# Performance work log

Hardware: AMD Instinct MI355X
Metric: run time of the kernel (lower is better)

## Reference

```python
import jax, jax.numpy as jnp
import numpy as np

LN_EPS = 1e-6
L2_EPS = 1e-12


def _l2_normalize(v):
    # tf.nn.l2_normalize: v * rsqrt(max(sum(v^2), eps))
    ss = jnp.sum(v * v, axis=-1, keepdims=True)
    return v * jax.lax.rsqrt(jnp.maximum(ss, L2_EPS))


def setup_inputs() -> dict:
    key = jax.random.key(0)
    k1, k2, k3 = jax.random.split(key, 3)
    B, S, D, V = 4, 2048, 1024, 16384
    x = jax.random.normal(k1, (B, S, D), dtype=jnp.float32)
    dict_w = jax.random.normal(k2, (V, D), dtype=jnp.float32) * (2.0 / (V + D)) ** 0.5  # glorot_normal
    ln_gamma = jnp.ones((D,), dtype=jnp.float32)
    ln_beta = jnp.zeros((D,), dtype=jnp.float32)
    o_w = jax.random.normal(k3, (D, D), dtype=jnp.float32) * (2.0 / (D + D)) ** 0.5
    return {"x": x, "dict_w": dict_w, "ln_gamma": ln_gamma, "ln_beta": ln_beta, "o_w": o_w}


def reference(x, dict_w, ln_gamma, ln_beta, o_w):
    # cosine-sim codebook lookup
    q = _l2_normalize(x)                      # [B,S,D]
    k = _l2_normalize(dict_w)                 # [V,D]
    sim = jnp.einsum('bsd,vd->bsv', q, k)     # [B,S,V]
    word_idx = jnp.argmax(sim, axis=-1)       # [B,S] int
    word_sim = jnp.max(sim, axis=-1)          # [B,S]
    z = dict_w[word_idx]                      # gather codebook rows [B,S,D]
    # straight-through estimator
    e = jax.lax.stop_gradient(z - x) + x
    # layernorm (eps=1e-6)
    mu = jnp.mean(e, axis=-1, keepdims=True)
    var = jnp.mean(jnp.square(e - mu), axis=-1, keepdims=True)
    e_ln = (e - mu) * jax.lax.rsqrt(var + LN_EPS) * ln_gamma + ln_beta
    # output projection (no bias)
    out = jnp.einsum('bsd,de->bse', e_ln, o_w)
    return word_idx, word_sim, out
```

## Files before the change

kernel.cpp:

```cpp
#include <hip/hip_runtime.h>
#include <math.h>

#define D 1024
#define V 16384
#define NROWS 8192
#define NCAND 256
#define DELTA 0.15f

typedef __bf16 bf16_t;
typedef bf16_t bf16x8 __attribute__((ext_vector_type(8)));
typedef float f32x4 __attribute__((ext_vector_type(4)));
typedef int i32x4 __attribute__((ext_vector_type(4)));

__device__ __forceinline__ unsigned int sortable_key(float v) {
    unsigned int b = __float_as_uint(v);
    return (b & 0x80000000u) ? ~b : (b | 0x80000000u);
}
__device__ __forceinline__ float unkey(unsigned int key) {
    unsigned int b = (key & 0x80000000u) ? (key & 0x7FFFFFFFu) : ~key;
    return __uint_as_float(b);
}
__device__ __forceinline__ void split4(float4 v, uint2& hw, uint2& lw) {
    unsigned int u0 = __float_as_uint(v.x), u1 = __float_as_uint(v.y);
    unsigned int u2 = __float_as_uint(v.z), u3 = __float_as_uint(v.w);
    float l0 = v.x - __uint_as_float(u0 & 0xFFFF0000u);
    float l1 = v.y - __uint_as_float(u1 & 0xFFFF0000u);
    float l2 = v.z - __uint_as_float(u2 & 0xFFFF0000u);
    float l3 = v.w - __uint_as_float(u3 & 0xFFFF0000u);
    hw.x = (u0 >> 16) | (u1 & 0xFFFF0000u);
    hw.y = (u2 >> 16) | (u3 & 0xFFFF0000u);
    lw.x = (__float_as_uint(l0) >> 16) | (__float_as_uint(l1) & 0xFFFF0000u);
    lw.y = (__float_as_uint(l2) >> 16) | (__float_as_uint(l3) & 0xFFFF0000u);
}

__device__ __forceinline__ void gload16(const unsigned char* g, unsigned char* s) {
    __builtin_amdgcn_global_load_lds((const __attribute__((address_space(1))) void*)g,
                                     (__attribute__((address_space(3))) void*)s,
                                     16, 0, 0);
}

__global__ __launch_bounds__(256) void prep_kernel(const float* __restrict__ W,
                                                   const float* __restrict__ X,
                                                   float* __restrict__ RK,
                                                   float* __restrict__ RQ,
                                                   float* __restrict__ SA,
                                                   float* __restrict__ SB,
                                                   float* __restrict__ RKS,
                                                   unsigned int* __restrict__ packed,
                                                   unsigned int* __restrict__ count) {
    int tid = threadIdx.x;
    int row = blockIdx.x * 4 + (tid >> 6);
    int lane = tid & 63;
    const float* src = (row < V) ? (W + (size_t)row * D) : (X + (size_t)(row - V) * D);
    const float4* p = (const float4*)src;
    float ss = 0.f, am = 0.f;
#pragma unroll
    for (int i = 0; i < 4; ++i) {
        float4 v = p[lane + 64 * i];
        ss += v.x * v.x + v.y * v.y + v.z * v.z + v.w * v.w;
        am = fmaxf(am, fmaxf(fmaxf(fabsf(v.x), fabsf(v.y)), fmaxf(fabsf(v.z), fabsf(v.w))));
    }
#pragma unroll
    for (int m = 32; m >= 1; m >>= 1) {
        ss += __shfl_xor(ss, m, 64);
        am = fmaxf(am, __shfl_xor(am, m, 64));
    }
    if (lane == 0) {
        float rk = rsqrtf(fmaxf(ss, 1e-12f));
        float s = am * (1.f / 127.f);
        if (row < V) {
            RK[row] = rk;
            SB[row] = s;
            RKS[row] = rk * s;
        } else {
            RQ[row - V] = rk;
            SA[row - V] = s;
            packed[row - V] = 0u;
            count[row - V] = 0u;
        }
    }
}

__global__ __launch_bounds__(256) void pack_i8_kernel(const float* __restrict__ src,
                                                      const float* __restrict__ S,
                                                      unsigned char* __restrict__ dst) {
    int tid = threadIdx.x;
    int row = blockIdx.x;
    int k0 = tid * 4;
    float4 v = *((const float4*)(src + (size_t)row * D) + tid);
    float s = S[row];
    float inv = (s > 0.f) ? (1.f / s) : 0.f;
    int q0 = (int)rintf(v.x * inv), q1 = (int)rintf(v.y * inv);
    int q2 = (int)rintf(v.z * inv), q3 = (int)rintf(v.w * inv);
    q0 = q0 > 127 ? 127 : (q0 < -127 ? -127 : q0);
    q1 = q1 > 127 ? 127 : (q1 < -127 ? -127 : q1);
    q2 = q2 > 127 ? 127 : (q2 < -127 ? -127 : q2);
    q3 = q3 > 127 ? 127 : (q3 < -127 ? -127 : q3);
    unsigned int word = (unsigned int)(q0 & 0xFF) | ((unsigned int)(q1 & 0xFF) << 8) |
                        ((unsigned int)(q2 & 0xFF) << 16) | ((unsigned int)(q3 & 0xFF) << 24);
    int kc = k0 >> 6, kk = k0 & 63;
    int lane = (row & 15) | ((kk >> 4) << 4);
    int j0 = kk & 15;
    size_t idx = ((size_t)(row >> 4) * 16 + kc) * 1024 + lane * 16 + j0;
    *(unsigned int*)(dst + idx) = word;
}

__global__ __launch_bounds__(256, 2) void gemm1_kernel(const unsigned char* __restrict__ Xq,
                                                       const unsigned char* __restrict__ Wq,
                                                       const float* __restrict__ SA,
                                                       const float* __restrict__ RKS,
                                                       unsigned int* __restrict__ packed,
                                                       unsigned int* __restrict__ count,
                                                       ushort* __restrict__ candCol,
                                                       int colBase, int perX) {
    __shared__ __align__(16) unsigned char lds[49152];
    __shared__ float red[128][2];
    __shared__ float gthr[128];

    const int tid = threadIdx.x;
    const int l = tid & 63;
    const int w = tid >> 6;
    const int wy = w >> 1, wx = w & 1;
    const int lin = blockIdx.x;
    const int x = lin & 7;
    const int j = lin >> 3;
    const int rt = j / perX;
    const int ctl = x * perX + (j - rt * perX);
    const int rowBase = rt * 128;
    const int cwLocal = ctl * 256;

    i32x4 acc[4][8];
#pragma unroll
    for (int mt = 0; mt < 4; ++mt)
#pragma unroll
        for (int nt = 0; nt < 8; ++nt) acc[mt][nt] = (i32x4)0;

    const unsigned char* As = Xq + ((size_t)(rt * 8) * 16) * 1024;
    const unsigned char* Bs = Wq + ((size_t)((colBase >> 4) + ctl * 16) * 16) * 1024;

#pragma unroll 1
    for (int kc = 0; kc < 16; kc += 2) {
#pragma unroll
        for (int i = 0; i < 2; ++i) {
            int u = 2 * w + i;
#pragma unroll
            for (int jj = 0; jj < 2; ++jj)
                gload16(As + ((size_t)(u * 16 + kc + jj)) * 1024 + l * 16,
                        lds + (u * 2 + jj) * 1024);
        }
#pragma unroll
        for (int i = 0; i < 4; ++i) {
            int u = 4 * w + i;
#pragma unroll
            for (int jj = 0; jj < 2; ++jj)
                gload16(Bs + ((size_t)(u * 16 + kc + jj)) * 1024 + l * 16,
                        lds + 16384 + (u * 2 + jj) * 1024);
        }
        __syncthreads();
#pragma unroll
        for (int jj = 0; jj < 2; ++jj) {
            i32x4 af[4], bf[8];
#pragma unroll
            for (int mi = 0; mi < 4; ++mi)
                af[mi] = *(const i32x4*)(lds + ((wy * 4 + mi) * 2 + jj) * 1024 + l * 16);
#pragma unroll
            for (int nt = 0; nt < 8; ++nt)
                bf[nt] = *(const i32x4*)(lds + 16384 + ((wx * 8 + nt) * 2 + jj) * 1024 + l * 16);
#pragma unroll
            for (int nt = 0; nt < 8; ++nt)
#pragma unroll
                for (int mi = 0; mi < 4; ++mi)
                    acc[mi][nt] = __builtin_amdgcn_mfma_i32_16x16x64_i8(af[mi], bf[nt], acc[mi][nt], 0, 0, 0);
        }
        __syncthreads();
    }

    const int q = l >> 4, c = l & 15;
    float rk_l[8];
#pragma unroll
    for (int nt = 0; nt < 8; ++nt) rk_l[nt] = RKS[colBase + cwLocal + wx * 128 + nt * 16 + c];
#pragma unroll
    for (int mt = 0; mt < 4; ++mt) {
#pragma unroll
        for (int r = 0; r < 4; ++r) {
            int lrow = wy * 64 + mt * 16 + q * 4 + r;
            float sa = SA[rowBase + lrow];
            float vmax = -1e30f;
#pragma unroll
            for (int nt = 0; nt < 8; ++nt)
                vmax = fmaxf(vmax, (float)acc[mt][nt][r] * sa * rk_l[nt]);
#pragma unroll
            for (int m = 1; m < 16; m <<= 1)
                vmax = fmaxf(vmax, __shfl_xor(vmax, m, 64));
            if (c == 0) red[lrow][wx] = vmax;
        }
    }
    __syncthreads();
    if (tid < 128) {
        float a = fmaxf(red[tid][0], red[tid][1]);
        unsigned int k = sortable_key(a);
        unsigned int old = atomicMax(packed + (rowBase + tid), k);
        unsigned int g = (old > k) ? old : k;
        gthr[tid] = unkey(g) - DELTA;
    }
    __syncthreads();
#pragma unroll
    for (int mt = 0; mt < 4; ++mt) {
#pragma unroll
        for (int r = 0; r < 4; ++r) {
            int lrow = wy * 64 + mt * 16 + q * 4 + r;
            float thr = gthr[lrow];
            int grow = rowBase + lrow;
            float sa = SA[grow];
#pragma unroll
            for (int nt = 0; nt < 8; ++nt) {
                float v = (float)acc[mt][nt][r] * sa * rk_l[nt];
                if (v >= thr) {
                    unsigned int slot = atomicAdd(count + grow, 1u);
                    if (slot < NCAND) {
                        int col = colBase + cwLocal + wx * 128 + nt * 16 + c;
                        candCol[(size_t)grow * NCAND + slot] = (ushort)col;
                    }
                }
            }
        }
    }
}

__global__ __launch_bounds__(256) void rescore_kernel(const float* __restrict__ X,
                                                      const float* __restrict__ W,
                                                      const float* __restrict__ RK,
                                                      const float* __restrict__ RQ,
                                                      const unsigned int* __restrict__ count,
                                                      const ushort* __restrict__ candCol,
                                                      float* __restrict__ outIdx,
                                                      float* __restrict__ outSim,
                                                      int* __restrict__ idxArr,
                                                      float* __restrict__ MU,
                                                      float* __restrict__ RS) {
    int wave = threadIdx.x >> 6, l = threadIdx.x & 63;
    int row = blockIdx.x * 4 + wave;
    unsigned int n = count[row];
    if (n > NCAND) n = NCAND;
    const float4* X4 = (const float4*)X + (size_t)row * 256;
    unsigned long long best = 0;
    for (unsigned int i = 0; i < n; ++i) {
        int col = (int)candCol[(size_t)row * NCAND + i];
        const float4* W4 = (const float4*)W + (size_t)col * 256;
        float s = 0.f;
#pragma unroll
        for (int jj = 0; jj < 4; ++jj) {
            float4 a = X4[jj * 64 + l];
            float4 b = W4[jj * 64 + l];
            s += a.x * b.x + a.y * b.y + a.z * b.z + a.w * b.w;
        }
#pragma unroll
        for (int m = 32; m >= 1; m >>= 1) s += __shfl_xor(s, m, 64);
        float v = s * RK[col];
        unsigned long long pk = ((unsigned long long)sortable_key(v) << 32) |
                                (unsigned long long)(~(unsigned int)col);
        if (pk > best) best = pk;
    }
    int idx = (int)(~(unsigned int)(best & 0xFFFFFFFFull)) & 0xFFFF;
    const float4* Z4 = (const float4*)W + (size_t)idx * 256;
    float s = 0.f, s2 = 0.f;
#pragma unroll
    for (int jj = 0; jj < 4; ++jj) {
        float4 a = X4[jj * 64 + l];
        float4 z = Z4[jj * 64 + l];
        float4 e;
        e.x = (z.x - a.x) + a.x;
        e.y = (z.y - a.y) + a.y;
        e.z = (z.z - a.z) + a.z;
        e.w = (z.w - a.w) + a.w;
        s  += e.x + e.y + e.z + e.w;
        s2 += e.x * e.x + e.y * e.y + e.z * e.z + e.w * e.w;
    }
#pragma unroll
    for (int m = 32; m >= 1; m >>= 1) {
        s  += __shfl_xor(s, m, 64);
        s2 += __shfl_xor(s2, m, 64);
    }
    if (l == 0) {
        outIdx[row] = (float)idx;
        outSim[row] = unkey((unsigned int)(best >> 32)) * RQ[row];
        idxArr[row] = idx;
        float mean = s * (1.f / D);
        float var  = s2 * (1.f / D) - mean * mean;
        MU[row] = mean;
        RS[row] = rsqrtf(var + 1e-6f);
    }
}

__global__ __launch_bounds__(256, 2) void gemm2_kernel(const float* __restrict__ X,
                                                       const float* __restrict__ W,
                                                       const int* __restrict__ idxArr,
                                                       const float* __restrict__ MU,
                                                       const float* __restrict__ RS,
                                                       const float* __restrict__ gamma,
                                                       const float* __restrict__ beta,
                                                       const float* __restrict__ B,
                                                       float* __restrict__ Out) {
    __shared__ ushort Ah[2][8][64][8];
    __shared__ ushort Al[2][8][64][8];
    __shared__ ushort Bh2[2][8][64][8];
    __shared__ ushort Bl2[2][8][64][8];
    __shared__ float Gs[1024];
    __shared__ float Bt[1024];

    const int tid = threadIdx.x;
    const int l = tid & 63;
    const int wave = tid >> 6;
    const int wy = wave >> 1, wx = wave & 1;
    const int rowBase = blockIdx.y * 128;
    const int nBase   = blockIdx.x * 128;

    *(float4*)&Gs[tid * 4] = *(const float4*)(gamma + tid * 4);
    *(float4*)&Bt[tid * 4] = *(const float4*)(beta + tid * 4);

    f32x4 acc[4][4];
#pragma unroll
    for (int mt = 0; mt < 4; ++mt)
#pragma unroll
        for (int nt = 0; nt < 4; ++nt) acc[mt][nt] = (f32x4)0.f;

    const int srow = tid >> 3, skq = tid & 7;
    const int sn = tid & 127, sdq = tid >> 7;
    int aidx[4];
    float amu[4], ars[4];
#pragma unroll
    for (int i = 0; i < 4; ++i) {
        int grow = rowBase + srow + i * 32;
        aidx[i] = idxArr[grow];
        amu[i] = MU[grow];
        ars[i] = RS[grow];
    }

    __syncthreads();

    float4 pz[4], pxv[4], pbv[4];
#pragma unroll
    for (int i = 0; i < 4; ++i) {
        int col = skq * 4;
        pz[i]  = *(const float4*)(W + (size_t)aidx[i] * D + col);
        pxv[i] = *(const float4*)(X + (size_t)(rowBase + srow + i * 32) * D + col);
    }
#pragma unroll
    for (int i = 0; i < 4; ++i) {
        const float* bp = B + (size_t)((sdq + i * 2) * 4) * D + nBase + sn;
        pbv[i] = {bp[0], bp[D], bp[2 * D], bp[3 * D]};
    }

    for (int kc = 0; kc < 32; ++kc) {
        const int bsel = kc & 1;
#pragma unroll
        for (int i = 0; i < 4; ++i) {
            int row = srow + i * 32;
            int col = kc * 32 + skq * 4;
            float4 z = pz[i], xv = pxv[i];
            float4 g  = *(const float4*)&Gs[col];
            float4 bb = *(const float4*)&Bt[col];
            float4 a;
            a.x = (((z.x - xv.x) + xv.x) - amu[i]) * ars[i] * g.x + bb.x;
            a.y = (((z.y - xv.y) + xv.y) - amu[i]) * ars[i] * g.y + bb.y;
            a.z = (((z.z - xv.z) + xv.z) - amu[i]) * ars[i] * g.z + bb.z;
            a.w = (((z.w - xv.w) + xv.w) - amu[i]) * ars[i] * g.w + bb.w;
            uint2 hw, lw;
            split4(a, hw, lw);
            int tile = row >> 4;
            int lf = (row & 15) | ((skq >> 1) << 4);
            int j0 = (skq & 1) * 4;
            *(uint2*)&Ah[bsel][tile][lf][j0] = hw;
            *(uint2*)&Al[bsel][tile][lf][j0] = lw;
        }
#pragma unroll
        for (int i = 0; i < 4; ++i) {
            int dq = sdq + i * 2;
            uint2 hw, lw;
            split4(pbv[i], hw, lw);
            int tile = sn >> 4;
            int lf = (sn & 15) | ((dq >> 1) << 4);
            int j0 = (dq & 1) * 4;
            *(uint2*)&Bh2[bsel][tile][lf][j0] = hw;
            *(uint2*)&Bl2[bsel][tile][lf][j0] = lw;
        }
        __syncthreads();
        float4 pzn[4], pxvn[4], pbvn[4];
        if (kc < 31) {
#pragma unroll
            for (int i = 0; i < 4; ++i) {
                int col = (kc + 1) * 32 + skq * 4;
                pzn[i]  = *(const float4*)(W + (size_t)aidx[i] * D + col);
                pxvn[i] = *(const float4*)(X + (size_t)(rowBase + srow + i * 32) * D + col);
            }
#pragma unroll
            for (int i = 0; i < 4; ++i) {
                const float* bp = B + (size_t)((kc + 1) * 32 + (sdq + i * 2) * 4) * D + nBase + sn;
                pbvn[i] = {bp[0], bp[D], bp[2 * D], bp[3 * D]};
            }
        }
        bf16x8 fah[4], fal[4];
#pragma unroll
        for (int mt = 0; mt < 4; ++mt) {
            fah[mt] = *(const bf16x8*)&Ah[bsel][wy * 4 + mt][l][0];
            fal[mt] = *(const bf16x8*)&Al[bsel][wy * 4 + mt][l][0];
        }
#pragma unroll
        for (int nt = 0; nt < 4; ++nt) {
            bf16x8 bh = *(const bf16x8*)&Bh2[bsel][wx * 4 + nt][l][0];
            bf16x8 bl = *(const bf16x8*)&Bl2[bsel][wx * 4 + nt][l][0];
#pragma unroll
            for (int mt = 0; mt < 4; ++mt) {
                acc[mt][nt] = __builtin_amdgcn_mfma_f32_16x16x32_bf16(fah[mt], bh, acc[mt][nt], 0, 0, 0);
                acc[mt][nt] = __builtin_amdgcn_mfma_f32_16x16x32_bf16(fah[mt], bl, acc[mt][nt], 0, 0, 0);
                acc[mt][nt] = __builtin_amdgcn_mfma_f32_16x16x32_bf16(fal[mt], bh, acc[mt][nt], 0, 0, 0);
            }
        }
        if (kc < 31) {
#pragma unroll
            for (int i = 0; i < 4; ++i) {
                pz[i] = pzn[i]; pxv[i] = pxvn[i]; pbv[i] = pbvn[i];
            }
        }
    }

    const int q = l >> 4, c = l & 15;
#pragma unroll
    for (int mt = 0; mt < 4; ++mt)
#pragma unroll
        for (int nt = 0; nt < 4; ++nt)
#pragma unroll
            for (int r = 0; r < 4; ++r) {
                int grow = rowBase + wy * 64 + mt * 16 + q * 4 + r;
                int gcol = nBase + wx * 64 + nt * 16 + c;
                Out[(size_t)grow * D + gcol] = acc[mt][nt][r];
            }
}

extern "C" void kernel_launch(void* const* d_in, const int* in_sizes, int n_in,
                              void* d_out, int out_size, void* d_ws, size_t ws_size,
                              hipStream_t stream) {
    const float* X     = (const float*)d_in[0];
    const float* W     = (const float*)d_in[1];
    const float* gamma = (const float*)d_in[2];
    const float* beta  = (const float*)d_in[3];
    const float* OW    = (const float*)d_in[4];

    float* out    = (float*)d_out;
    float* outIdx = out;
    float* outSim = out + NROWS;
    float* outO   = out + 2 * NROWS;

    unsigned char* Xq8 = (unsigned char*)outO;
    unsigned char* Wq8 = Xq8 + (size_t)NROWS * D;
    ushort* candCol = (ushort*)(Wq8 + (size_t)V * D);
    unsigned int* count = (unsigned int*)(candCol + (size_t)NROWS * NCAND);
    float* SA  = (float*)(count + NROWS);
    float* SB  = SA + NROWS;
    float* RKS = SB + V;

    unsigned int* packed = (unsigned int*)d_ws;
    float* RK     = (float*)(packed + NROWS);
    float* RQ     = RK + V;
    float* MU     = RQ + NROWS;
    float* RS     = MU + NROWS;
    int*   idxArr = (int*)(RS + NROWS);

    hipLaunchKernelGGL(prep_kernel, dim3((V + NROWS) / 4), dim3(256), 0, stream,
                       W, X, RK, RQ, SA, SB, RKS, packed, count);
    hipLaunchKernelGGL(pack_i8_kernel, dim3(NROWS), dim3(256), 0, stream, X, SA, Xq8);
    hipLaunchKernelGGL(pack_i8_kernel, dim3(V), dim3(256), 0, stream, W, SB, Wq8);

    for (int ch = 0; ch < 2; ++ch) {
        int colBase = ch * 8192;
        int perX = (8192 / 256) / 8;
        hipLaunchKernelGGL(gemm1_kernel, dim3((NROWS / 128) * (8192 / 256)), dim3(256), 0, stream,
                           Xq8, Wq8, SA, RKS, packed, count, candCol, colBase, perX);
    }

    hipLaunchKernelGGL(rescore_kernel, dim3(NROWS / 4), dim3(256), 0, stream,
                       X, W, RK, RQ, count, candCol, outIdx, outSim, idxArr, MU, RS);
    hipLaunchKernelGGL(gemm2_kernel, dim3(D / 128, NROWS / 128), dim3(256), 0, stream,
                       X, W, idxArr, MU, RS, gamma, beta, OW, outO);
}
```

Before: 499.5 us.

## Fuse prep into int8 pack, double-buffer gemm1 loads, single full-width launch

Folds the norm/absmax prep and int8 quantization into one packq kernel per matrix, so each input row is read once instead of twice. The int8 GEMM now processes one k-chunk per iteration with double-buffered LDS, issuing the next chunk's global-to-LDS loads before the current chunk's MFMAs. The two half-width gemm1 launches become a single launch covering all columns. This trades a block-level reduction and extra syncs in the pack kernel, and a different block-to-tile mapping, for fewer passes over memory and better overlap of loads with compute.

```diff
diff --git a/kernel.cpp b/kernel.cpp
--- a/kernel.cpp
+++ b/kernel.cpp
@@ -39,57 +39,46 @@
                                      16, 0, 0);
 }
 
-__global__ __launch_bounds__(256) void prep_kernel(const float* __restrict__ W,
-                                                   const float* __restrict__ X,
-                                                   float* __restrict__ RK,
-                                                   float* __restrict__ RQ,
-                                                   float* __restrict__ SA,
-                                                   float* __restrict__ SB,
-                                                   float* __restrict__ RKS,
-                                                   unsigned int* __restrict__ packed,
-                                                   unsigned int* __restrict__ count) {
+__global__ __launch_bounds__(256) void packq_kernel(const float* __restrict__ src,
+                                                    unsigned char* __restrict__ dst,
+                                                    float* __restrict__ oRK,
+                                                    float* __restrict__ oS,
+                                                    unsigned int* __restrict__ packed,
+                                                    unsigned int* __restrict__ count,
+                                                    int isX) {
+    __shared__ float rss[4], ram[4];
+    __shared__ float binv;
     int tid = threadIdx.x;
-    int row = blockIdx.x * 4 + (tid >> 6);
-    int lane = tid & 63;
-    const float* src = (row < V) ? (W + (size_t)row * D) : (X + (size_t)(row - V) * D);
-    const float4* p = (const float4*)src;
-    float ss = 0.f, am = 0.f;
-#pragma unroll
-    for (int i = 0; i < 4; ++i) {
-        float4 v = p[lane + 64 * i];
-        ss += v.x * v.x + v.y * v.y + v.z * v.z + v.w * v.w;
-        am = fmaxf(am, fmaxf(fmaxf(fabsf(v.x), fabsf(v.y)), fmaxf(fabsf(v.z), fabsf(v.w))));
-    }
+    int row = blockIdx.x;
+    float4 v = *((const float4*)(src + (size_t)row * D) + tid);
+    float ss = v.x * v.x + v.y * v.y + v.z * v.z + v.w * v.w;
+    float am = fmaxf(fmaxf(fabsf(v.x), fabsf(v.y)), fmaxf(fabsf(v.z), fabsf(v.w)));
 #pragma unroll
     for (int m = 32; m >= 1; m >>= 1) {
         ss += __shfl_xor(ss, m, 64);
         am = fmaxf(am, __shfl_xor(am, m, 64));
     }
-    if (lane == 0) {
-        float rk = rsqrtf(fmaxf(ss, 1e-12f));
-        float s = am * (1.f / 127.f);
-        if (row < V) {
-            RK[row] = rk;
-            SB[row] = s;
-            RKS[row] = rk * s;
+    int wv = tid >> 6, ln = tid & 63;
+    if (ln == 0) { rss[wv] = ss; ram[wv] = am; }
+    __syncthreads();
+    if (tid == 0) {
+        float S = (rss[0] + rss[1]) + (rss[2] + rss[3]);
+        float A = fmaxf(fmaxf(ram[0], ram[1]), fmaxf(ram[2], ram[3]));
+        float rk = rsqrtf(fmaxf(S, 1e-12f));
+        float s = A * (1.f / 127.f);
+        if (isX) {
+            oRK[row] = rk;
+            oS[row]  = s;
+            packed[row] = 0u;
+            count[row]  = 0u;
         } else {
-            RQ[row - V] = rk;
-            SA[row - V] = s;
-            packed[row - V] = 0u;
-            count[row - V] = 0u;
-        }
-    }
-}
-
-__global__ __launch_bounds__(256) void pack_i8_kernel(const float* __restrict__ src,
-                                                      const float* __restrict__ S,
-                                                      unsigned char* __restrict__ dst) {
-    int tid = threadIdx.x;
-    int row = blockIdx.x;
-    int k0 = tid * 4;
-    float4 v = *((const float4*)(src + (size_t)row * D) + tid);
-    float s = S[row];
-    float inv = (s > 0.f) ? (1.f / s) : 0.f;
+            oRK[row] = rk;
+            oS[row]  = rk * s;
+        }
+        binv = (s > 0.f) ? (1.f / s) : 0.f;
+    }
+    __syncthreads();
+    float inv = binv;
     int q0 = (int)rintf(v.x * inv), q1 = (int)rintf(v.y * inv);
     int q2 = (int)rintf(v.z * inv), q3 = (int)rintf(v.w * inv);
     q0 = q0 > 127 ? 127 : (q0 < -127 ? -127 : q0);
@@ -98,6 +87,7 @@
     q3 = q3 > 127 ? 127 : (q3 < -127 ? -127 : q3);
     unsigned int word = (unsigned int)(q0 & 0xFF) | ((unsigned int)(q1 & 0xFF) << 8) |
                         ((unsigned int)(q2 & 0xFF) << 16) | ((unsigned int)(q3 & 0xFF) << 24);
+    int k0 = tid * 4;
     int kc = k0 >> 6, kk = k0 & 63;
     int lane = (row & 15) | ((kk >> 4) << 4);
     int j0 = kk & 15;
@@ -111,8 +101,7 @@
                                                        const float* __restrict__ RKS,
                                                        unsigned int* __restrict__ packed,
                                                        unsigned int* __restrict__ count,
-                                                       ushort* __restrict__ candCol,
-                                                       int colBase, int perX) {
+                                                       ushort* __restrict__ candCol) {
     __shared__ __align__(16) unsigned char lds[49152];
     __shared__ float red[128][2];
     __shared__ float gthr[128];
@@ -124,10 +113,10 @@
     const int lin = blockIdx.x;
     const int x = lin & 7;
     const int j = lin >> 3;
-    const int rt = j / perX;
-    const int ctl = x * perX + (j - rt * perX);
+    const int rt = j >> 3;
+    const int ctl = x * 8 + (j & 7);
     const int rowBase = rt * 128;
-    const int cwLocal = ctl * 256;
+    const int colBase = ctl * 256;
 
     i32x4 acc[4][8];
 #pragma unroll
@@ -136,49 +125,58 @@
         for (int nt = 0; nt < 8; ++nt) acc[mt][nt] = (i32x4)0;
 
     const unsigned char* As = Xq + ((size_t)(rt * 8) * 16) * 1024;
-    const unsigned char* Bs = Wq + ((size_t)((colBase >> 4) + ctl * 16) * 16) * 1024;
+    const unsigned char* Bs = Wq + ((size_t)(ctl * 16) * 16) * 1024;
+
+#pragma unroll
+    for (int i = 0; i < 2; ++i) {
+        int u = 2 * w + i;
+        gload16(As + ((size_t)(u * 16 + 0)) * 1024 + l * 16, lds + u * 1024);
+    }
+#pragma unroll
+    for (int i = 0; i < 4; ++i) {
+        int u = 4 * w + i;
+        gload16(Bs + ((size_t)(u * 16 + 0)) * 1024 + l * 16, lds + 8192 + u * 1024);
+    }
+    __syncthreads();
 
 #pragma unroll 1
-    for (int kc = 0; kc < 16; kc += 2) {
-#pragma unroll
-        for (int i = 0; i < 2; ++i) {
-            int u = 2 * w + i;
-#pragma unroll
-            for (int jj = 0; jj < 2; ++jj)
-                gload16(As + ((size_t)(u * 16 + kc + jj)) * 1024 + l * 16,
-                        lds + (u * 2 + jj) * 1024);
-        }
-#pragma unroll
-        for (int i = 0; i < 4; ++i) {
-            int u = 4 * w + i;
-#pragma unroll
-            for (int jj = 0; jj < 2; ++jj)
-                gload16(Bs + ((size_t)(u * 16 + kc + jj)) * 1024 + l * 16,
-                        lds + 16384 + (u * 2 + jj) * 1024);
-        }
-        __syncthreads();
-#pragma unroll
-        for (int jj = 0; jj < 2; ++jj) {
-            i32x4 af[4], bf[8];
+    for (int kc = 0; kc < 16; ++kc) {
+        const int cur = (kc & 1) * 24576;
+        const int nxt = ((kc & 1) ^ 1) * 24576;
+        if (kc + 1 < 16) {
+#pragma unroll
+            for (int i = 0; i < 2; ++i) {
+                int u = 2 * w + i;
+                gload16(As + ((size_t)(u * 16 + kc + 1)) * 1024 + l * 16,
+                        lds + nxt + u * 1024);
+            }
+#pragma unroll
+            for (int i = 0; i < 4; ++i) {
+                int u = 4 * w + i;
+                gload16(Bs + ((size_t)(u * 16 + kc + 1)) * 1024 + l * 16,
+                        lds + nxt + 8192 + u * 1024);
+            }
+        }
+        __builtin_amdgcn_sched_barrier(0);
+        i32x4 af[4], bf[8];
+#pragma unroll
+        for (int mi = 0; mi < 4; ++mi)
+            af[mi] = *(const i32x4*)(lds + cur + (wy * 4 + mi) * 1024 + l * 16);
+#pragma unroll
+        for (int nt = 0; nt < 8; ++nt)
+            bf[nt] = *(const i32x4*)(lds + cur + 8192 + (wx * 8 + nt) * 1024 + l * 16);
+#pragma unroll
+        for (int nt = 0; nt < 8; ++nt)
 #pragma unroll
             for (int mi = 0; mi < 4; ++mi)
-                af[mi] = *(const i32x4*)(lds + ((wy * 4 + mi) * 2 + jj) * 1024 + l * 16);
-#pragma unroll
-            for (int nt = 0; nt < 8; ++nt)
-                bf[nt] = *(const i32x4*)(lds + 16384 + ((wx * 8 + nt) * 2 + jj) * 1024 + l * 16);
-#pragma unroll
-            for (int nt = 0; nt < 8; ++nt)
-#pragma unroll
-                for (int mi = 0; mi < 4; ++mi)
-                    acc[mi][nt] = __builtin_amdgcn_mfma_i32_16x16x64_i8(af[mi], bf[nt], acc[mi][nt], 0, 0, 0);
-        }
+                acc[mi][nt] = __builtin_amdgcn_mfma_i32_16x16x64_i8(af[mi], bf[nt], acc[mi][nt], 0, 0, 0);
         __syncthreads();
     }
 
     const int q = l >> 4, c = l & 15;
     float rk_l[8];
 #pragma unroll
-    for (int nt = 0; nt < 8; ++nt) rk_l[nt] = RKS[colBase + cwLocal + wx * 128 + nt * 16 + c];
+    for (int nt = 0; nt < 8; ++nt) rk_l[nt] = RKS[colBase + wx * 128 + nt * 16 + c];
 #pragma unroll
     for (int mt = 0; mt < 4; ++mt) {
 #pragma unroll
@@ -218,7 +216,7 @@
                 if (v >= thr) {
                     unsigned int slot = atomicAdd(count + grow, 1u);
                     if (slot < NCAND) {
-                        int col = colBase + cwLocal + wx * 128 + nt * 16 + c;
+                        int col = colBase + wx * 128 + nt * 16 + c;
                         candCol[(size_t)grow * NCAND + slot] = (ushort)col;
                     }
                 }
@@ -456,8 +454,7 @@
     ushort* candCol = (ushort*)(Wq8 + (size_t)V * D);
     unsigned int* count = (unsigned int*)(candCol + (size_t)NROWS * NCAND);
     float* SA  = (float*)(count + NROWS);
-    float* SB  = SA + NROWS;
-    float* RKS = SB + V;
+    float* RKS = SA + NROWS;
 
     unsigned int* packed = (unsigned int*)d_ws;
     float* RK     = (float*)(packed + NROWS);
@@ -466,17 +463,13 @@
     float* RS     = MU + NROWS;
     int*   idxArr = (int*)(RS + NROWS);
 
-    hipLaunchKernelGGL(prep_kernel, dim3((V + NROWS) / 4), dim3(256), 0, stream,
-                       W, X, RK, RQ, SA, SB, RKS, packed, count);
-    hipLaunchKernelGGL(pack_i8_kernel, dim3(NROWS), dim3(256), 0, stream, X, SA, Xq8);
-    hipLaunchKernelGGL(pack_i8_kernel, dim3(V), dim3(256), 0, stream, W, SB, Wq8);
-
-    for (int ch = 0; ch < 2; ++ch) {
-        int colBase = ch * 8192;
-        int perX = (8192 / 256) / 8;
-        hipLaunchKernelGGL(gemm1_kernel, dim3((NROWS / 128) * (8192 / 256)), dim3(256), 0, stream,
-                           Xq8, Wq8, SA, RKS, packed, count, candCol, colBase, perX);
-    }
+    hipLaunchKernelGGL(packq_kernel, dim3(V), dim3(256), 0, stream,
+                       W, Wq8, RK, RKS, (unsigned int*)nullptr, (unsigned int*)nullptr, 0);
+    hipLaunchKernelGGL(packq_kernel, dim3(NROWS), dim3(256), 0, stream,
+                       X, Xq8, RQ, SA, packed, count, 1);
+
+    hipLaunchKernelGGL(gemm1_kernel, dim3((NROWS / 128) * (V / 256)), dim3(256), 0, stream,
+                       Xq8, Wq8, SA, RKS, packed, count, candCol);
 
     hipLaunchKernelGGL(rescore_kernel, dim3(NROWS / 4), dim3(256), 0, stream,
                        X, W, RK, RQ, count, candCol, outIdx, outSim, idxArr, MU, RS);
```

Result: no change. 491.2 us (-1.7%).
